# Optimization experiments

Hardware: AMD Instinct MI355X
Metric: run time of the kernel (lower is better)

Reference implementation:

```python
import jax, jax.numpy as jnp
import numpy as np

N_NODES = 100000
N_EDGES = 1600000
IN_DIM = 64
EDGE_DIM = 8
H1, H2 = 128, 64
FEAT = 2 * IN_DIM + EDGE_DIM  # 136


def setup_inputs() -> dict:
    key = jax.random.key(0)
    ks = jax.random.split(key, 9)
    z = jax.random.normal(ks[0], (N_NODES, IN_DIM), dtype=jnp.float32)
    edge_index = jax.random.randint(ks[1], (2, N_EDGES), 0, N_NODES, dtype=jnp.int64)
    edge_attr = jax.random.normal(ks[2], (N_EDGES, EDGE_DIM), dtype=jnp.float32)
    # MLP params (Linear stores weight as [out, in]; we keep [in, out] for x @ W)
    def lin(k, fan_in, fan_out):
        bound = 1.0 / np.sqrt(fan_in)
        kw, kb = jax.random.split(k)
        W = jax.random.uniform(kw, (fan_in, fan_out), minval=-bound, maxval=bound, dtype=jnp.float32)
        b = jax.random.uniform(kb, (fan_out,), minval=-bound, maxval=bound, dtype=jnp.float32)
        return W, b
    W1, b1 = lin(ks[3], FEAT, H1)
    W2, b2 = lin(ks[4], H1, H2)
    W3, b3 = lin(ks[5], H2, 1)
    return {"z": z, "edge_index": edge_index, "edge_attr": edge_attr,
            "W1": W1, "b1": b1, "W2": W2, "b2": b2, "W3": W3, "b3": b3}


def reference(z, edge_index, edge_attr, W1, b1, W2, b2, W3, b3):
    src, dst = edge_index[0], edge_index[1]
    # gather node embeddings per edge and concat with edge attributes: [E, 2*D+A]
    feat = jnp.concatenate([z[src], z[dst], edge_attr], axis=-1)
    h = jax.nn.relu(feat @ W1 + b1)   # Dropout is identity in eval mode
    h = jax.nn.relu(h @ W2 + b2)
    logits = (h @ W3 + b3).squeeze(-1)  # [E]
    return logits
```

## Files before the change

### kernel.cpp

```cpp
#include <hip/hip_runtime.h>
#include <hip/hip_bf16.h>
#include <stdint.h>
#include <stddef.h>

#define NODES 100000
#define EDGES 1600000
#define NCHUNK 6250
#define EDGE_GRID 3125
#define NTILES 6250

typedef float f4 __attribute__((ext_vector_type(4)));
typedef float f32x4 __attribute__((ext_vector_type(4)));
typedef short s8v __attribute__((ext_vector_type(8)));
typedef unsigned short u16x8 __attribute__((ext_vector_type(8)));

__device__ __forceinline__ float bf2f(unsigned short u) {
  union { unsigned int i; float f; } v; v.i = ((unsigned int)u) << 16; return v.f;
}
__device__ __forceinline__ unsigned short f2bf(float f) {
  union { float f; unsigned int i; } v; v.f = f;
  return (unsigned short)((v.i + 0x7FFFu + ((v.i >> 16) & 1u)) >> 16);
}
__device__ __forceinline__ short f2bf_hw(float x) {
  __hip_bfloat16 h = __float2bfloat16(x);
  union { __hip_bfloat16 h; short s; } u; u.h = h; return u.s;
}

__device__ __forceinline__ int pqperm(int jj) {
  return (jj & 0x60) | ((jj & 0x0C) << 1) | ((jj & 0x10) >> 2) | (jj & 3);
}

__global__ __launch_bounds__(256) void node_pq_mfma(
    const float* __restrict__ z, const float* __restrict__ W1,
    const float* __restrict__ b1, unsigned short* __restrict__ PQ) {
  const int t = threadIdx.x;
  const int lane = t & 63;
  const int w = t >> 6;
  const int r = lane & 15, g = lane >> 4;
  const int tile = blockIdx.x * 4 + w;
  if (tile >= NTILES) return;
  const int n0 = tile * 16;

  s8v a_hi[2], a_lo[2];
#pragma unroll
  for (int kt = 0; kt < 2; ++kt) {
    const f4* zp = (const f4*)(z + (size_t)(n0 + r) * 64 + 32 * kt + 8 * g);
    f4 z0 = zp[0], z1 = zp[1];
    float zv[8] = {z0[0], z0[1], z0[2], z0[3], z1[0], z1[1], z1[2], z1[3]};
    s8v hi, lo;
#pragma unroll
    for (int jx = 0; jx < 8; ++jx) {
      short h = f2bf_hw(zv[jx]);
      hi[jx] = h;
      lo[jx] = f2bf_hw(zv[jx] - bf2f((unsigned short)h));
    }
    a_hi[kt] = hi; a_lo[kt] = lo;
  }

#pragma unroll 1
  for (int nt = 0; nt < 16; ++nt) {
    const int col = (nt & 7) * 16 + r;
    const int rowbase = (nt < 8) ? 0 : 64;
    const float init = (nt < 8) ? b1[col] : 0.f;
    f32x4 acc = {init, init, init, init};
#pragma unroll
    for (int kt = 0; kt < 2; ++kt) {
      s8v whi, wlo;
#pragma unroll
      for (int jx = 0; jx < 8; ++jx) {
        float wv = W1[(size_t)(rowbase + 32 * kt + 8 * g + jx) * 128 + col];
        short h = f2bf_hw(wv);
        whi[jx] = h;
        wlo[jx] = f2bf_hw(wv - bf2f((unsigned short)h));
      }
      acc = __builtin_amdgcn_mfma_f32_16x16x32_bf16(a_hi[kt], whi, acc, 0, 0, 0);
      acc = __builtin_amdgcn_mfma_f32_16x16x32_bf16(a_lo[kt], whi, acc, 0, 0, 0);
      acc = __builtin_amdgcn_mfma_f32_16x16x32_bf16(a_hi[kt], wlo, acc, 0, 0, 0);
    }
    const int outcol = (nt < 8) ? pqperm(col) : (128 + pqperm(col));
#pragma unroll
    for (int reg = 0; reg < 4; ++reg)
      PQ[(size_t)(n0 + 4 * g + reg) * 256 + outcol] = f2bf(acc[reg]);
  }
}

__global__ __launch_bounds__(256) void edge_mfma_kernel(
    const int* __restrict__ eidx, const float* __restrict__ eattr,
    const float* __restrict__ W1, const float* __restrict__ W2,
    const float* __restrict__ b2, const float* __restrict__ W3,
    const float* __restrict__ b3,
    const unsigned short* __restrict__ PQ, float* __restrict__ out) {
  const int t = threadIdx.x;
  const int lane = t & 63;
  const int w = t >> 6;
  const int r = lane & 15;
  const int g = lane >> 4;

  s8v bfrag[4][4];
#pragma unroll
  for (int kt = 0; kt < 4; ++kt)
#pragma unroll
    for (int nt = 0; nt < 4; ++nt) {
      s8v f;
#pragma unroll
      for (int jx = 0; jx < 8; ++jx) {
        int h = jx >> 2, jp = jx & 3;
        int jjv = 32 * kt + 16 * h + 4 * g + jp;
        f[jx] = (short)f2bf(W2[(size_t)jjv * 64 + nt * 16 + r]);
      }
      bfrag[kt][nt] = f;
    }
  s8v w1cf[8];
#pragma unroll
  for (int mt = 0; mt < 8; ++mt) {
    s8v f = {0, 0, 0, 0, 0, 0, 0, 0};
    if (g == 0) {
#pragma unroll
      for (int jx = 0; jx < 8; ++jx)
        f[jx] = (short)f2bf(W1[(size_t)(128 + jx) * 128 + 16 * mt + r]);
    }
    w1cf[mt] = f;
  }
  float b2v[4], w3v[4];
#pragma unroll
  for (int nt = 0; nt < 4; ++nt) { b2v[nt] = b2[nt * 16 + r]; w3v[nt] = W3[nt * 16 + r]; }
  const float bias3 = b3[0];
  const f32x4 zc = {0.f, 0.f, 0.f, 0.f};

#pragma unroll 1
  for (int chunk = blockIdx.x; chunk < NCHUNK; chunk += EDGE_GRID) {
    const int ebase = chunk * 256 + w * 64;
    const int src_all = eidx[ebase + lane];
    const int dst_all = eidx[EDGES + ebase + lane];
    unsigned int ea_pk[4];
    {
      const f4* eap = (const f4*)(eattr + (size_t)(ebase + lane) * 8);
      f4 a0 = eap[0], a1 = eap[1];
      ea_pk[0] = (unsigned int)(unsigned short)f2bf_hw(a0[0]) |
                 ((unsigned int)(unsigned short)f2bf_hw(a0[1]) << 16);
      ea_pk[1] = (unsigned int)(unsigned short)f2bf_hw(a0[2]) |
                 ((unsigned int)(unsigned short)f2bf_hw(a0[3]) << 16);
      ea_pk[2] = (unsigned int)(unsigned short)f2bf_hw(a1[0]) |
                 ((unsigned int)(unsigned short)f2bf_hw(a1[1]) << 16);
      ea_pk[3] = (unsigned int)(unsigned short)f2bf_hw(a1[2]) |
                 ((unsigned int)(unsigned short)f2bf_hw(a1[3]) << 16);
    }

    int srcv[4], dstv[4];
    s8v eafv[4];
#pragma unroll
    for (int st = 0; st < 4; ++st) {
      const int idx = st * 16 + r;
      srcv[st] = __shfl(src_all, idx, 64);
      dstv[st] = __shfl(dst_all, idx, 64);
      union { unsigned int u[4]; s8v v; } eu;
#pragma unroll
      for (int c = 0; c < 4; ++c) eu.u[c] = (unsigned int)__shfl((int)ea_pk[c], idx, 64);
      eafv[st] = eu.v;
    }

    u16x8 p[4][4], q[4][4];
#define PQ_LOAD(s)                                                             \
    {                                                                          \
      const unsigned short* Pb = PQ + (size_t)srcv[s] * 256 + 8 * g;           \
      const unsigned short* Qb = PQ + (size_t)dstv[s] * 256 + 128 + 8 * g;     \
      _Pragma("unroll")                                                        \
      for (int kt = 0; kt < 4; ++kt) {                                         \
        p[s][kt] = *(const u16x8*)(Pb + 32 * kt);                              \
        q[s][kt] = *(const u16x8*)(Qb + 32 * kt);                              \
      }                                                                        \
    }

#define PQ_COMPUTE(s)                                                          \
    {                                                                          \
      const int e0 = ebase + (s) * 16;                                         \
      f32x4 acc[4] = {zc, zc, zc, zc};                                         \
      _Pragma("unroll")                                                        \
      for (int kt = 0; kt < 4; ++kt) {                                         \
        f32x4 E0 = __builtin_amdgcn_mfma_f32_16x16x32_bf16(w1cf[2 * kt], eafv[s], zc, 0, 0, 0); \
        f32x4 E1 = __builtin_amdgcn_mfma_f32_16x16x32_bf16(w1cf[2 * kt + 1], eafv[s], zc, 0, 0, 0); \
        s8v af;                                                                \
        _Pragma("unroll")                                                      \
        for (int jp = 0; jp < 4; ++jp) {                                       \
          float s0 = bf2f(p[s][kt][jp]) + bf2f(q[s][kt][jp]) + E0[jp];         \
          af[jp] = f2bf_hw(fmaxf(s0, 0.f));                                    \
          float s1 = bf2f(p[s][kt][4 + jp]) + bf2f(q[s][kt][4 + jp]) + E1[jp]; \
          af[4 + jp] = f2bf_hw(fmaxf(s1, 0.f));                                \
        }                                                                      \
        _Pragma("unroll")                                                      \
        for (int nt = 0; nt < 4; ++nt)                                         \
          acc[nt] = __builtin_amdgcn_mfma_f32_16x16x32_bf16(af, bfrag[kt][nt], acc[nt], 0, 0, 0); \
      }                                                                        \
      float pr0 = 0.f, pr1 = 0.f, pr2 = 0.f, pr3 = 0.f;                        \
      _Pragma("unroll")                                                        \
      for (int nt = 0; nt < 4; ++nt) {                                         \
        pr0 = fmaf(fmaxf(acc[nt][0] + b2v[nt], 0.f), w3v[nt], pr0);            \
        pr1 = fmaf(fmaxf(acc[nt][1] + b2v[nt], 0.f), w3v[nt], pr1);            \
        pr2 = fmaf(fmaxf(acc[nt][2] + b2v[nt], 0.f), w3v[nt], pr2);            \
        pr3 = fmaf(fmaxf(acc[nt][3] + b2v[nt], 0.f), w3v[nt], pr3);            \
      }                                                                        \
      _Pragma("unroll")                                                        \
      for (int m = 1; m < 16; m <<= 1) {                                       \
        pr0 += __shfl_xor(pr0, m, 64);                                         \
        pr1 += __shfl_xor(pr1, m, 64);                                         \
        pr2 += __shfl_xor(pr2, m, 64);                                         \
        pr3 += __shfl_xor(pr3, m, 64);                                         \
      }                                                                        \
      if (r < 4) {                                                             \
        float v = (r == 0) ? pr0 : (r == 1) ? pr1 : (r == 2) ? pr2 : pr3;      \
        out[e0 + 4 * g + r] = v + bias3;                                       \
      }                                                                        \
    }

    PQ_LOAD(0)
    PQ_LOAD(1)
    PQ_COMPUTE(0)
    PQ_LOAD(2)
    PQ_COMPUTE(1)
    PQ_LOAD(3)
    PQ_COMPUTE(2)
    PQ_COMPUTE(3)
#undef PQ_LOAD
#undef PQ_COMPUTE
  }
}

extern "C" void kernel_launch(void* const* d_in, const int* in_sizes, int n_in,
                              void* d_out, int out_size, void* d_ws, size_t ws_size,
                              hipStream_t stream) {
  const float* z     = (const float*)d_in[0];
  const int*   eidx  = (const int*)d_in[1];
  const float* eattr = (const float*)d_in[2];
  const float* W1    = (const float*)d_in[3];
  const float* b1    = (const float*)d_in[4];
  const float* W2    = (const float*)d_in[5];
  const float* b2    = (const float*)d_in[6];
  const float* W3    = (const float*)d_in[7];
  const float* b3    = (const float*)d_in[8];
  float* out = (float*)d_out;

  unsigned short* PQ = (unsigned short*)d_ws;
  node_pq_mfma<<<(NTILES + 3) / 4, 256, 0, stream>>>(z, W1, b1, PQ);
  edge_mfma_kernel<<<EDGE_GRID, 256, 0, stream>>>(
      eidx, eattr, W1, W2, b2, W3, b3, PQ, out);
}
```

Baseline: 175.6 us.

## Software-pipeline edge chunks across iterations with persistent fewer blocks

The edge kernel now launches 1250 blocks, each handling exactly 5 chunks, instead of 3125 blocks striding over chunks. While the current chunk is still computing, each iteration prefetches the next chunk's indices and edge attributes, converts and shuffles them, and issues its first PQ gather. This is meant to hide gather latency at chunk boundaries. It also adds launch bounds asking for 4 waves per SIMD, which raises register pressure and adds eafv swap bookkeeping, with the risk of lower occupancy or spills.

```diff
diff --git a/kernel.cpp b/kernel.cpp
--- a/kernel.cpp
+++ b/kernel.cpp
@@ -6,7 +6,8 @@
 #define NODES 100000
 #define EDGES 1600000
 #define NCHUNK 6250
-#define EDGE_GRID 3125
+#define EDGE_GRID 1250
+#define CPB 5
 #define NTILES 6250
 
 typedef float f4 __attribute__((ext_vector_type(4)));
@@ -84,7 +85,7 @@
   }
 }
 
-__global__ __launch_bounds__(256) void edge_mfma_kernel(
+__global__ __launch_bounds__(256, 4) void edge_mfma_kernel(
     const int* __restrict__ eidx, const float* __restrict__ eattr,
     const float* __restrict__ W1, const float* __restrict__ W2,
     const float* __restrict__ b2, const float* __restrict__ W3,
@@ -127,39 +128,22 @@
   const float bias3 = b3[0];
   const f32x4 zc = {0.f, 0.f, 0.f, 0.f};
 
-#pragma unroll 1
-  for (int chunk = blockIdx.x; chunk < NCHUNK; chunk += EDGE_GRID) {
-    const int ebase = chunk * 256 + w * 64;
-    const int src_all = eidx[ebase + lane];
-    const int dst_all = eidx[EDGES + ebase + lane];
-    unsigned int ea_pk[4];
-    {
-      const f4* eap = (const f4*)(eattr + (size_t)(ebase + lane) * 8);
-      f4 a0 = eap[0], a1 = eap[1];
-      ea_pk[0] = (unsigned int)(unsigned short)f2bf_hw(a0[0]) |
-                 ((unsigned int)(unsigned short)f2bf_hw(a0[1]) << 16);
-      ea_pk[1] = (unsigned int)(unsigned short)f2bf_hw(a0[2]) |
-                 ((unsigned int)(unsigned short)f2bf_hw(a0[3]) << 16);
-      ea_pk[2] = (unsigned int)(unsigned short)f2bf_hw(a1[0]) |
-                 ((unsigned int)(unsigned short)f2bf_hw(a1[1]) << 16);
-      ea_pk[3] = (unsigned int)(unsigned short)f2bf_hw(a1[2]) |
-                 ((unsigned int)(unsigned short)f2bf_hw(a1[3]) << 16);
-    }
-
-    int srcv[4], dstv[4];
-    s8v eafv[4];
-#pragma unroll
-    for (int st = 0; st < 4; ++st) {
-      const int idx = st * 16 + r;
-      srcv[st] = __shfl(src_all, idx, 64);
-      dstv[st] = __shfl(dst_all, idx, 64);
-      union { unsigned int u[4]; s8v v; } eu;
-#pragma unroll
-      for (int c = 0; c < 4; ++c) eu.u[c] = (unsigned int)__shfl((int)ea_pk[c], idx, 64);
-      eafv[st] = eu.v;
-    }
-
-    u16x8 p[4][4], q[4][4];
+  int srcv[4], dstv[4];
+  s8v eafv[4];
+  u16x8 p[4][4], q[4][4];
+
+#define PACK_EA(pk, a0, a1)                                                    \
+    {                                                                          \
+      pk[0] = (unsigned int)(unsigned short)f2bf_hw(a0[0]) |                   \
+              ((unsigned int)(unsigned short)f2bf_hw(a0[1]) << 16);            \
+      pk[1] = (unsigned int)(unsigned short)f2bf_hw(a0[2]) |                   \
+              ((unsigned int)(unsigned short)f2bf_hw(a0[3]) << 16);            \
+      pk[2] = (unsigned int)(unsigned short)f2bf_hw(a1[0]) |                   \
+              ((unsigned int)(unsigned short)f2bf_hw(a1[1]) << 16);            \
+      pk[3] = (unsigned int)(unsigned short)f2bf_hw(a1[2]) |                   \
+              ((unsigned int)(unsigned short)f2bf_hw(a1[3]) << 16);            \
+    }
+
 #define PQ_LOAD(s)                                                             \
     {                                                                          \
       const unsigned short* Pb = PQ + (size_t)srcv[s] * 256 + 8 * g;           \
@@ -171,9 +155,9 @@
       }                                                                        \
     }
 
-#define PQ_COMPUTE(s)                                                          \
+#define PQ_COMPUTE(s, EB)                                                      \
     {                                                                          \
-      const int e0 = ebase + (s) * 16;                                         \
+      const int e0 = (EB) + (s) * 16;                                          \
       f32x4 acc[4] = {zc, zc, zc, zc};                                         \
       _Pragma("unroll")                                                        \
       for (int kt = 0; kt < 4; ++kt) {                                         \
@@ -212,17 +196,69 @@
       }                                                                        \
     }
 
+  {
+    const int ebase0 = blockIdx.x * 256 + w * 64;
+    const int s_all = eidx[ebase0 + lane];
+    const int d_all = eidx[EDGES + ebase0 + lane];
+    const f4* eap = (const f4*)(eattr + (size_t)(ebase0 + lane) * 8);
+    f4 a0 = eap[0], a1 = eap[1];
+    unsigned int pk[4];
+    PACK_EA(pk, a0, a1)
+#pragma unroll
+    for (int st = 0; st < 4; ++st) {
+      const int idx = st * 16 + r;
+      srcv[st] = __shfl(s_all, idx, 64);
+      dstv[st] = __shfl(d_all, idx, 64);
+      union { unsigned int u[4]; s8v v; } eu;
+#pragma unroll
+      for (int c = 0; c < 4; ++c) eu.u[c] = (unsigned int)__shfl((int)pk[c], idx, 64);
+      eafv[st] = eu.v;
+    }
     PQ_LOAD(0)
+  }
+
+#pragma unroll 1
+  for (int it = 0; it < CPB; ++it) {
+    const int ebase = (blockIdx.x + it * EDGE_GRID) * 256 + w * 64;
+    const int nbase = ebase + EDGE_GRID * 256;
+    int nsrc = 0, ndst = 0;
+    f4 na0 = {0.f, 0.f, 0.f, 0.f}, na1 = {0.f, 0.f, 0.f, 0.f};
+    if (it < CPB - 1) {
+      nsrc = eidx[nbase + lane];
+      ndst = eidx[EDGES + nbase + lane];
+      const f4* neap = (const f4*)(eattr + (size_t)(nbase + lane) * 8);
+      na0 = neap[0]; na1 = neap[1];
+    }
     PQ_LOAD(1)
-    PQ_COMPUTE(0)
+    PQ_COMPUTE(0, ebase)
     PQ_LOAD(2)
-    PQ_COMPUTE(1)
+    PQ_COMPUTE(1, ebase)
     PQ_LOAD(3)
-    PQ_COMPUTE(2)
-    PQ_COMPUTE(3)
+    PQ_COMPUTE(2, ebase)
+    s8v tmp3 = eafv[3];
+    if (it < CPB - 1) {
+      unsigned int npk[4];
+      PACK_EA(npk, na0, na1)
+#pragma unroll
+      for (int st = 0; st < 4; ++st) {
+        const int idx = st * 16 + r;
+        srcv[st] = __shfl(nsrc, idx, 64);
+        dstv[st] = __shfl(ndst, idx, 64);
+        union { unsigned int u[4]; s8v v; } eu;
+#pragma unroll
+        for (int c = 0; c < 4; ++c) eu.u[c] = (unsigned int)__shfl((int)npk[c], idx, 64);
+        if (st == 3) { s8v sw = eafv[3]; eafv[3] = eu.v; tmp3 = sw; }
+        else eafv[st] = eu.v;
+      }
+      { s8v cur = tmp3; tmp3 = eafv[3]; eafv[3] = cur; }
+      PQ_LOAD(0)
+    }
+    PQ_COMPUTE(3, ebase)
+    if (it < CPB - 1) eafv[3] = tmp3;
+  }
 #undef PQ_LOAD
 #undef PQ_COMPUTE
-  }
+#undef PACK_EA
 }
 
 extern "C" void kernel_launch(void* const* d_in, const int* in_sizes, int n_in,
```

Result: slower. 596.2 us (+239.6%).
